# Performance work log

Measured on AMD Instinct MI355X. Metric: run time of the kernel, lower is better.

## Reference

```python
import jax, jax.numpy as jnp
import numpy as np
import math

B, S, D, H = 2, 2048, 1024, 16
DH = D // H  # head_size = 64


def setup_inputs() -> dict:
    key = jax.random.key(0)
    ks = jax.random.split(key, 11)
    s = 0.02
    return {
        "queries": jax.random.normal(ks[0], (B, S, D), jnp.float32),
        "keys": jax.random.normal(ks[1], (B, S, D), jnp.float32),
        "values": jax.random.normal(ks[2], (B, S, D), jnp.float32),
        # nn.Linear weights: y = x @ W.T + b, W has shape (out, in)
        "W_Q": jax.random.normal(ks[3], (D, D), jnp.float32) * s,
        "b_Q": jax.random.normal(ks[4], (D,), jnp.float32) * s,
        "W_K": jax.random.normal(ks[5], (D, D), jnp.float32) * s,
        "b_K": jax.random.normal(ks[6], (D,), jnp.float32) * s,
        "W_V": jax.random.normal(ks[7], (D, D), jnp.float32) * s,
        "b_V": jax.random.normal(ks[8], (D,), jnp.float32) * s,
        "W_O": jax.random.normal(ks[9], (D, D), jnp.float32) * s,
        "b_O": jax.random.normal(ks[10], (D,), jnp.float32) * s,
    }


def _split_heads(x):
    # (B, S, H*DH) -> (B, H, S, DH); torch.chunk+stack == reshape+transpose
    b, s, _ = x.shape
    return x.reshape(b, s, H, DH).transpose(0, 2, 1, 3)


def reference(queries, keys, values, W_Q, b_Q, W_K, b_K, W_V, b_V, W_O, b_O):
    q = _split_heads(queries @ W_Q.T + b_Q)  # (B,H,S,DH)
    k = _split_heads(keys @ W_K.T + b_K)
    v = _split_heads(values @ W_V.T + b_V)

    scale = 1.0 / math.sqrt(DH)
    scores = jnp.einsum("bhqd,bhkd->bhqk", q, k) * scale  # (B,H,S,S)
    causal = jnp.tril(jnp.ones((S, S), dtype=bool))  # allow j <= i (causal)
    scores = jnp.where(causal, scores, -jnp.inf)
    weights = jax.nn.softmax(scores, axis=-1)

    attended = jnp.einsum("bhqk,bhkd->bhqd", weights, v)  # (B,H,S,DH)
    merged = attended.transpose(0, 2, 1, 3).reshape(B, S, D)  # merge_heads
    return merged @ W_O.T + b_O
```

## Files before the change

### kernel.cpp

```cpp
#include <hip/hip_runtime.h>


typedef __bf16 bf16x8 __attribute__((ext_vector_type(8)));
typedef float  f32x4  __attribute__((ext_vector_type(4)));

#define B_  2
#define S_  2048
#define D_  1024
#define H_  16
#define DH_ 64

#define NEG_ 1.0e30f
#define M2_  5.77078016f
#define QSCALE_ 0.18033688f

#if __has_builtin(__builtin_amdgcn_exp2f)
#define EXP2(x) __builtin_amdgcn_exp2f(x)
#else
#define EXP2(x) __builtin_exp2f(x)
#endif

__device__ __forceinline__ void load_lds16(const __bf16* g, __bf16* lds_base) {
    __builtin_amdgcn_global_load_lds(
        (const __attribute__((address_space(1))) void*)g,
        (__attribute__((address_space(3))) void*)lds_base,
        16, 0, 0);
}

__device__ __forceinline__ bf16x8 cvt8(const float* __restrict__ p) {
    const float4 a = *(const float4*)p;
    const float4 b = *(const float4*)(p + 4);
    bf16x8 r;
    r[0] = (__bf16)a.x; r[1] = (__bf16)a.y; r[2] = (__bf16)a.z; r[3] = (__bf16)a.w;
    r[4] = (__bf16)b.x; r[5] = (__bf16)b.y; r[6] = (__bf16)b.z; r[7] = (__bf16)b.w;
    return r;
}

__global__ void cvt_kernel(const float* __restrict__ q, const float* __restrict__ k,
                           const float* __restrict__ v,
                           const float* __restrict__ wq, const float* __restrict__ wk,
                           const float* __restrict__ wv, const float* __restrict__ wo,
                           __bf16* __restrict__ qb, __bf16* __restrict__ kb,
                           __bf16* __restrict__ vb,
                           __bf16* __restrict__ wqb, __bf16* __restrict__ wkb,
                           __bf16* __restrict__ wvb, __bf16* __restrict__ wob) {
    const int z = blockIdx.z;
    const float* src; __bf16* dst; size_t n;
    switch (z) {
        case 0: src = q;  dst = qb;  n = (size_t)B_ * S_ * D_; break;
        case 1: src = k;  dst = kb;  n = (size_t)B_ * S_ * D_; break;
        case 2: src = v;  dst = vb;  n = (size_t)B_ * S_ * D_; break;
        case 3: src = wq; dst = wqb; n = (size_t)D_ * D_; break;
        case 4: src = wk; dst = wkb; n = (size_t)D_ * D_; break;
        case 5: src = wv; dst = wvb; n = (size_t)D_ * D_; break;
        default: src = wo; dst = wob; n = (size_t)D_ * D_; break;
    }
    const size_t i = ((size_t)blockIdx.x * 256 + threadIdx.x) * 8;
    if (i >= n) return;
    *(bf16x8*)(dst + i) = cvt8(src + i);
}

__device__ __forceinline__ void gemm128_bf(const __bf16* __restrict__ X,
                                           const __bf16* __restrict__ W,
                                           int m0, int n0, int K,
                                           __bf16* As, __bf16* Bs,
                                           f32x4 acc[4][4]) {
    const int tid  = threadIdx.x;
    const int wave = tid >> 6, lane = tid & 63;
    const int row  = lane & 15, quad = lane >> 4;
    const int wm   = wave >> 1, wn = wave & 1;
    const int arow = lane >> 2;
    const int acol = (lane & 3) * 8;

    const f32x4 fzero = {0.f, 0.f, 0.f, 0.f};
#pragma unroll
    for (int mt = 0; mt < 4; ++mt)
#pragma unroll
        for (int nt = 0; nt < 4; ++nt) acc[mt][nt] = fzero;

    for (int k0 = 0; k0 < K; k0 += 32) {
#pragma unroll
        for (int c = 0; c < 2; ++c) {
            const int j = wave * 2 + c;
            load_lds16(X + (size_t)(m0 + j * 16 + arow) * K + k0 + acol, As + j * 512);
            load_lds16(W + (size_t)(n0 + j * 16 + arow) * K + k0 + acol, Bs + j * 512);
        }
        __syncthreads();
        bf16x8 af[4], bfv[4];
#pragma unroll
        for (int t = 0; t < 4; ++t) {
            af[t]  = *(const bf16x8*)(As + (wm * 64 + t * 16 + row) * 32 + quad * 8);
            bfv[t] = *(const bf16x8*)(Bs + (wn * 64 + t * 16 + row) * 32 + quad * 8);
        }
#pragma unroll
        for (int mt = 0; mt < 4; ++mt)
#pragma unroll
            for (int nt = 0; nt < 4; ++nt)
                acc[mt][nt] = __builtin_amdgcn_mfma_f32_16x16x32_bf16(
                    af[mt], bfv[nt], acc[mt][nt], 0, 0, 0);
        __syncthreads();
    }
}

__global__ void qkv_kernel(const __bf16* __restrict__ qb, const __bf16* __restrict__ kb,
                           const __bf16* __restrict__ vb,
                           const __bf16* __restrict__ wqb, const __bf16* __restrict__ wkb,
                           const __bf16* __restrict__ wvb,
                           const float* __restrict__ bq, const float* __restrict__ bk,
                           const float* __restrict__ bv,
                           __bf16* __restrict__ q_ws, __bf16* __restrict__ k_ws,
                           __bf16* __restrict__ v_ws) {
    __shared__ __align__(16) __bf16 As[128 * 32];
    __shared__ __align__(16) __bf16 Bs[128 * 32];
    const int mode = blockIdx.z;
    const __bf16* X    = mode == 0 ? qb : mode == 1 ? kb : vb;
    const __bf16* W    = mode == 0 ? wqb : mode == 1 ? wkb : wvb;
    const float*  bias = mode == 0 ? bq : mode == 1 ? bk : bv;
    const int m0 = blockIdx.y * 128, n0 = blockIdx.x * 128;

    f32x4 acc[4][4];
    gemm128_bf(X, W, m0, n0, D_, As, Bs, acc);

    const int tid = threadIdx.x;
    const int wave = tid >> 6, lane = tid & 63;
    const int row = lane & 15, quad = lane >> 4;
    const int wm = wave >> 1, wn = wave & 1;

#pragma unroll
    for (int nt = 0; nt < 4; ++nt) {
        const int n  = n0 + wn * 64 + nt * 16 + row;
        const float bf = bias[n];
        const int h = n >> 6, dh = n & 63;
#pragma unroll
        for (int mt = 0; mt < 4; ++mt) {
#pragma unroll
            for (int r = 0; r < 4; ++r) {
                const int m = m0 + wm * 64 + mt * 16 + quad * 4 + r;
                const int bb = m >> 11, s = m & (S_ - 1);
                const float val = acc[mt][nt][r] + bf;
                if (mode == 0)
                    q_ws[(((size_t)bb * H_ + h) * S_ + s) * DH_ + dh] = (__bf16)(val * QSCALE_);
                else if (mode == 1)
                    k_ws[(((size_t)bb * H_ + h) * S_ + s) * DH_ + dh] = (__bf16)val;
                else
                    v_ws[(((size_t)bb * H_ + h) * DH_ + dh) * S_ + s] = (__bf16)val;
            }
        }
    }
}

__global__ void attn_kernel(const __bf16* __restrict__ q_ws, const __bf16* __restrict__ k_ws,
                            const __bf16* __restrict__ v_ws, __bf16* __restrict__ att) {
    __shared__ __align__(16) __bf16 Ks[128 * 64];
    __shared__ __align__(16) __bf16 Vs[64 * 128];
    __shared__ __align__(16) __bf16 Ps[4 * 32 * 32];

    const int bh = blockIdx.x;
    const int qt = (S_ / 128 - 1) - blockIdx.y;
    const int tid = threadIdx.x, wave = tid >> 6, lane = tid & 63;
    const int row = lane & 15, quad = lane >> 4;

    const __bf16* Qg = q_ws + ((size_t)bh * S_ + qt * 128 + wave * 32) * DH_;
    const __bf16* Kg = k_ws + (size_t)bh * S_ * DH_;
    const __bf16* Vg = v_ws + (size_t)bh * DH_ * S_;
    __bf16* Pw = Ps + wave * 1024;

    bf16x8 qf[2][2];
#pragma unroll
    for (int mt = 0; mt < 2; ++mt)
#pragma unroll
        for (int ks = 0; ks < 2; ++ks)
            qf[mt][ks] = *(const bf16x8*)(Qg + (mt * 16 + row) * DH_ + ks * 32 + quad * 8);

    bf16x8 onesf;
#pragma unroll
    for (int i = 0; i < 8; ++i) onesf[i] = (__bf16)1.0f;

    const f32x4 fzero = {0.f, 0.f, 0.f, 0.f};
    f32x4 oacc[2][4];
    f32x4 lacc[2];
#pragma unroll
    for (int mt = 0; mt < 2; ++mt) {
#pragma unroll
        for (int dt = 0; dt < 4; ++dt) oacc[mt][dt] = fzero;
        lacc[mt] = fzero;
    }

    for (int kv = 0; kv <= qt; ++kv) {
#pragma unroll
        for (int c = 0; c < 4; ++c) {
            const int ck = wave * 4 + c;
            load_lds16(Kg + (size_t)kv * 128 * DH_ + ck * 512 + lane * 8, Ks + ck * 512);
            load_lds16(Vg + (size_t)(ck * 4 + (lane >> 4)) * S_ + kv * 128 + (lane & 15) * 8,
                       Vs + ck * 512);
        }
        __syncthreads();

        const bool diag = (kv == qt);
#pragma unroll
        for (int kc = 0; kc < 4; ++kc) {
            f32x4 s[2][2];
#pragma unroll
            for (int mt = 0; mt < 2; ++mt)
#pragma unroll
                for (int jn = 0; jn < 2; ++jn) s[mt][jn] = fzero;
#pragma unroll
            for (int jn = 0; jn < 2; ++jn) {
                const int nt = kc * 2 + jn;
                bf16x8 kf0 = *(const bf16x8*)(Ks + (nt * 16 + row) * DH_ + quad * 8);
                bf16x8 kf1 = *(const bf16x8*)(Ks + (nt * 16 + row) * DH_ + 32 + quad * 8);
#pragma unroll
                for (int mt = 0; mt < 2; ++mt) {
                    s[mt][jn] = __builtin_amdgcn_mfma_f32_16x16x32_bf16(qf[mt][0], kf0, s[mt][jn], 0, 0, 0);
                    s[mt][jn] = __builtin_amdgcn_mfma_f32_16x16x32_bf16(qf[mt][1], kf1, s[mt][jn], 0, 0, 0);
                }
            }

            if (diag) {
#pragma unroll
                for (int mt = 0; mt < 2; ++mt)
#pragma unroll
                    for (int jn = 0; jn < 2; ++jn) {
                        const int cloc = kc * 32 + jn * 16 + row;
#pragma unroll
                        for (int r = 0; r < 4; ++r) {
                            const int rloc = wave * 32 + mt * 16 + quad * 4 + r;
                            if (cloc > rloc) s[mt][jn][r] = -NEG_;
                        }
                    }
            }

#pragma unroll
            for (int mt = 0; mt < 2; ++mt)
#pragma unroll
                for (int r = 0; r < 4; ++r)
#pragma unroll
                    for (int jn = 0; jn < 2; ++jn) {
                        const float p = EXP2(s[mt][jn][r] - M2_);
                        Pw[(mt * 16 + quad * 4 + r) * 32 + jn * 16 + row] = (__bf16)p;
                    }

            bf16x8 pf0 = *(const bf16x8*)(Pw + (row) * 32 + quad * 8);
            bf16x8 pf1 = *(const bf16x8*)(Pw + (16 + row) * 32 + quad * 8);
#pragma unroll
            for (int dt = 0; dt < 4; ++dt) {
                bf16x8 vf = *(const bf16x8*)(Vs + (dt * 16 + row) * 128 + kc * 32 + quad * 8);
                oacc[0][dt] = __builtin_amdgcn_mfma_f32_16x16x32_bf16(pf0, vf, oacc[0][dt], 0, 0, 0);
                oacc[1][dt] = __builtin_amdgcn_mfma_f32_16x16x32_bf16(pf1, vf, oacc[1][dt], 0, 0, 0);
            }
            lacc[0] = __builtin_amdgcn_mfma_f32_16x16x32_bf16(pf0, onesf, lacc[0], 0, 0, 0);
            lacc[1] = __builtin_amdgcn_mfma_f32_16x16x32_bf16(pf1, onesf, lacc[1], 0, 0, 0);
        }
        __syncthreads();
    }

    const int b = bh >> 4, h = bh & 15;
#pragma unroll
    for (int mt = 0; mt < 2; ++mt) {
#pragma unroll
        for (int r = 0; r < 4; ++r) {
            const float inv = 1.f / lacc[mt][r];
            const int s = qt * 128 + wave * 32 + mt * 16 + quad * 4 + r;
#pragma unroll
            for (int dt = 0; dt < 4; ++dt) {
                att[((size_t)b * S_ + s) * D_ + h * DH_ + dt * 16 + row] =
                    (__bf16)(oacc[mt][dt][r] * inv);
            }
        }
    }
}

__global__ void oproj_kernel(const __bf16* __restrict__ attn, const __bf16* __restrict__ wob,
                             const float* __restrict__ bo, float* __restrict__ out) {
    __shared__ __align__(16) __bf16 As[128 * 32];
    __shared__ __align__(16) __bf16 Bs[128 * 32];
    const int m0 = blockIdx.y * 128, n0 = blockIdx.x * 128;

    f32x4 acc[4][4];
    gemm128_bf(attn, wob, m0, n0, D_, As, Bs, acc);

    const int tid = threadIdx.x;
    const int wave = tid >> 6, lane = tid & 63;
    const int row = lane & 15, quad = lane >> 4;
    const int wm = wave >> 1, wn = wave & 1;

#pragma unroll
    for (int nt = 0; nt < 4; ++nt) {
        const int n = n0 + wn * 64 + nt * 16 + row;
        const float bf = bo[n];
#pragma unroll
        for (int mt = 0; mt < 4; ++mt) {
#pragma unroll
            for (int r = 0; r < 4; ++r) {
                const int m = m0 + wm * 64 + mt * 16 + quad * 4 + r;
                out[(size_t)m * D_ + n] = acc[mt][nt][r] + bf;
            }
        }
    }
}

extern "C" void kernel_launch(void* const* d_in, const int* in_sizes, int n_in,
                              void* d_out, int out_size, void* d_ws, size_t ws_size,
                              hipStream_t stream) {
    const float* q_in = (const float*)d_in[0];
    const float* k_in = (const float*)d_in[1];
    const float* v_in = (const float*)d_in[2];
    const float* wq   = (const float*)d_in[3];
    const float* bq   = (const float*)d_in[4];
    const float* wk   = (const float*)d_in[5];
    const float* bk   = (const float*)d_in[6];
    const float* wv   = (const float*)d_in[7];
    const float* bv   = (const float*)d_in[8];
    const float* wo   = (const float*)d_in[9];
    const float* bo   = (const float*)d_in[10];

    char* ws = (char*)d_ws;
    const size_t MB = 1024 * 1024;
    __bf16* qb   = (__bf16*)(ws);
    __bf16* kb   = (__bf16*)(ws + 8 * MB);
    __bf16* vb   = (__bf16*)(ws + 16 * MB);
    __bf16* wqb  = (__bf16*)(ws + 24 * MB);
    __bf16* wkb  = (__bf16*)(ws + 26 * MB);
    __bf16* wvb  = (__bf16*)(ws + 28 * MB);
    __bf16* wob  = (__bf16*)(ws + 30 * MB);
    __bf16* q_ws = (__bf16*)(ws + 32 * MB);
    __bf16* k_ws = (__bf16*)(ws + 40 * MB);
    __bf16* v_ws = (__bf16*)(ws + 48 * MB);
    __bf16* attb = qb;
    float*  out  = (float*)d_out;

    cvt_kernel<<<dim3(2048, 1, 7), 256, 0, stream>>>(
        q_in, k_in, v_in, wq, wk, wv, wo, qb, kb, vb, wqb, wkb, wvb, wob);
    qkv_kernel<<<dim3(D_ / 128, (B_ * S_) / 128, 3), 256, 0, stream>>>(
        qb, kb, vb, wqb, wkb, wvb, bq, bk, bv, q_ws, k_ws, v_ws);
    attn_kernel<<<dim3(B_ * H_, S_ / 128), 256, 0, stream>>>(q_ws, k_ws, v_ws, attb);
    oproj_kernel<<<dim3(D_ / 128, (B_ * S_) / 128), 256, 0, stream>>>(attb, wob, bo, out);
}
```

Before: 242.6 us.

## Compute transposed scores to keep P in registers and skip masked diagonal tiles

The attention kernel now computes S^T = K·Q^T, so each lane's score fragment maps straight onto the A-operand layout of a 16x16x16 MFMA for P·V. That removes the LDS round-trip for P and the ones-vector MFMA used for row sums; row sums are instead kept as per-lane float accumulators and reduced with shuffles at the end. K and V tiles are staged into padded LDS with 4-byte global_load_lds to avoid bank conflicts. On the diagonal tile each wave processes only the key subtiles its causal mask can reach. The costs are 4x more small LDS-load instructions and a lower-throughput MFMA shape for P·V.

Result: slower. 255.9 us (+5.5%).

```diff
diff --git a/kernel.cpp b/kernel.cpp
--- a/kernel.cpp
+++ b/kernel.cpp
@@ -2,6 +2,8 @@
 
 
 typedef __bf16 bf16x8 __attribute__((ext_vector_type(8)));
+typedef __bf16 bf16x4 __attribute__((ext_vector_type(4)));
+typedef short  s16x4  __attribute__((ext_vector_type(4)));
 typedef float  f32x4  __attribute__((ext_vector_type(4)));
 
 #define B_  2
@@ -20,11 +22,26 @@
 #define EXP2(x) __builtin_exp2f(x)
 #endif
 
+__device__ __forceinline__ f32x4 mfma16x16(bf16x4 a, bf16x4 b, f32x4 c) {
+#if __has_builtin(__builtin_amdgcn_mfma_f32_16x16x16_bf16)
+    return __builtin_amdgcn_mfma_f32_16x16x16_bf16(a, b, c, 0, 0, 0);
+#else
+    return __builtin_amdgcn_mfma_f32_16x16x16bf16_1k(
+        __builtin_bit_cast(s16x4, a), __builtin_bit_cast(s16x4, b), c, 0, 0, 0);
+#endif
+}
+
 __device__ __forceinline__ void load_lds16(const __bf16* g, __bf16* lds_base) {
     __builtin_amdgcn_global_load_lds(
         (const __attribute__((address_space(1))) void*)g,
         (__attribute__((address_space(3))) void*)lds_base,
         16, 0, 0);
+}
+__device__ __forceinline__ void load_lds4(const __bf16* g, __bf16* lds_base) {
+    __builtin_amdgcn_global_load_lds(
+        (const __attribute__((address_space(1))) void*)g,
+        (__attribute__((address_space(3))) void*)lds_base,
+        4, 0, 0);
 }
 
 __device__ __forceinline__ bf16x8 cvt8(const float* __restrict__ p) {
@@ -149,11 +166,12 @@
     }
 }
 
+#define KSTR 136
+#define VSTR 136
 __global__ void attn_kernel(const __bf16* __restrict__ q_ws, const __bf16* __restrict__ k_ws,
                             const __bf16* __restrict__ v_ws, __bf16* __restrict__ att) {
-    __shared__ __align__(16) __bf16 Ks[128 * 64];
-    __shared__ __align__(16) __bf16 Vs[64 * 128];
-    __shared__ __align__(16) __bf16 Ps[4 * 32 * 32];
+    __shared__ __align__(16) __bf16 Ks[64 * KSTR];
+    __shared__ __align__(16) __bf16 Vs[64 * VSTR];
 
     const int bh = blockIdx.x;
     const int qt = (S_ / 128 - 1) - blockIdx.y;
@@ -163,108 +181,97 @@
     const __bf16* Qg = q_ws + ((size_t)bh * S_ + qt * 128 + wave * 32) * DH_;
     const __bf16* Kg = k_ws + (size_t)bh * S_ * DH_;
     const __bf16* Vg = v_ws + (size_t)bh * DH_ * S_;
-    __bf16* Pw = Ps + wave * 1024;
 
     bf16x8 qf[2][2];
 #pragma unroll
-    for (int mt = 0; mt < 2; ++mt)
+    for (int jq = 0; jq < 2; ++jq)
 #pragma unroll
         for (int ks = 0; ks < 2; ++ks)
-            qf[mt][ks] = *(const bf16x8*)(Qg + (mt * 16 + row) * DH_ + ks * 32 + quad * 8);
-
-    bf16x8 onesf;
-#pragma unroll
-    for (int i = 0; i < 8; ++i) onesf[i] = (__bf16)1.0f;
+            qf[jq][ks] = *(const bf16x8*)(Qg + (jq * 16 + row) * DH_ + ks * 32 + quad * 8);
 
     const f32x4 fzero = {0.f, 0.f, 0.f, 0.f};
     f32x4 oacc[2][4];
-    f32x4 lacc[2];
-#pragma unroll
-    for (int mt = 0; mt < 2; ++mt) {
-#pragma unroll
-        for (int dt = 0; dt < 4; ++dt) oacc[mt][dt] = fzero;
-        lacc[mt] = fzero;
-    }
+    float lsum[2] = {0.f, 0.f};
+#pragma unroll
+    for (int jq = 0; jq < 2; ++jq)
+#pragma unroll
+        for (int dt = 0; dt < 4; ++dt) oacc[jq][dt] = fzero;
+
+    const int kfbase = (row >> 1) * KSTR + (row & 1) * 64 + quad * 8;
+    const int vfbase = row * VSTR + quad * 4;
 
     for (int kv = 0; kv <= qt; ++kv) {
 #pragma unroll
-        for (int c = 0; c < 4; ++c) {
-            const int ck = wave * 4 + c;
-            load_lds16(Kg + (size_t)kv * 128 * DH_ + ck * 512 + lane * 8, Ks + ck * 512);
-            load_lds16(Vg + (size_t)(ck * 4 + (lane >> 4)) * S_ + kv * 128 + (lane & 15) * 8,
-                       Vs + ck * 512);
+        for (int c = 0; c < 16; ++c) {
+            const int g = wave * 16 + c;
+            load_lds4(Kg + (size_t)kv * 128 * DH_ + g * 128 + lane * 2, Ks + g * KSTR);
+            load_lds4(Vg + (size_t)g * S_ + kv * 128 + lane * 2, Vs + g * VSTR);
         }
         __syncthreads();
 
         const bool diag = (kv == qt);
-#pragma unroll
-        for (int kc = 0; kc < 4; ++kc) {
-            f32x4 s[2][2];
-#pragma unroll
-            for (int mt = 0; mt < 2; ++mt)
-#pragma unroll
-                for (int jn = 0; jn < 2; ++jn) s[mt][jn] = fzero;
-#pragma unroll
-            for (int jn = 0; jn < 2; ++jn) {
-                const int nt = kc * 2 + jn;
-                bf16x8 kf0 = *(const bf16x8*)(Ks + (nt * 16 + row) * DH_ + quad * 8);
-                bf16x8 kf1 = *(const bf16x8*)(Ks + (nt * 16 + row) * DH_ + 32 + quad * 8);
-#pragma unroll
-                for (int mt = 0; mt < 2; ++mt) {
-                    s[mt][jn] = __builtin_amdgcn_mfma_f32_16x16x32_bf16(qf[mt][0], kf0, s[mt][jn], 0, 0, 0);
-                    s[mt][jn] = __builtin_amdgcn_mfma_f32_16x16x32_bf16(qf[mt][1], kf1, s[mt][jn], 0, 0, 0);
+        const int nkt = diag ? (2 * wave + 2) : 8;
+
+        for (int kt = 0; kt < nkt; ++kt) {
+            bf16x8 kf0 = *(const bf16x8*)(Ks + kfbase + kt * 8 * KSTR);
+            bf16x8 kf1 = *(const bf16x8*)(Ks + kfbase + kt * 8 * KSTR + 32);
+            f32x4 s[2];
+#pragma unroll
+            for (int jq = 0; jq < 2; ++jq) {
+                s[jq] = __builtin_amdgcn_mfma_f32_16x16x32_bf16(kf0, qf[jq][0], fzero, 0, 0, 0);
+                s[jq] = __builtin_amdgcn_mfma_f32_16x16x32_bf16(kf1, qf[jq][1], s[jq], 0, 0, 0);
+            }
+
+            if (diag) {
+#pragma unroll
+                for (int jq = 0; jq < 2; ++jq) {
+                    const int q = wave * 32 + jq * 16 + row;
+#pragma unroll
+                    for (int r = 0; r < 4; ++r) {
+                        const int key = kt * 16 + quad * 4 + r;
+                        if (key > q) s[jq][r] = -NEG_;
+                    }
                 }
             }
 
-            if (diag) {
-#pragma unroll
-                for (int mt = 0; mt < 2; ++mt)
-#pragma unroll
-                    for (int jn = 0; jn < 2; ++jn) {
-                        const int cloc = kc * 32 + jn * 16 + row;
-#pragma unroll
-                        for (int r = 0; r < 4; ++r) {
-                            const int rloc = wave * 32 + mt * 16 + quad * 4 + r;
-                            if (cloc > rloc) s[mt][jn][r] = -NEG_;
-                        }
-                    }
-            }
-
-#pragma unroll
-            for (int mt = 0; mt < 2; ++mt)
-#pragma unroll
-                for (int r = 0; r < 4; ++r)
-#pragma unroll
-                    for (int jn = 0; jn < 2; ++jn) {
-                        const float p = EXP2(s[mt][jn][r] - M2_);
-                        Pw[(mt * 16 + quad * 4 + r) * 32 + jn * 16 + row] = (__bf16)p;
-                    }
-
-            bf16x8 pf0 = *(const bf16x8*)(Pw + (row) * 32 + quad * 8);
-            bf16x8 pf1 = *(const bf16x8*)(Pw + (16 + row) * 32 + quad * 8);
+            bf16x4 pa[2];
+#pragma unroll
+            for (int jq = 0; jq < 2; ++jq) {
+                float ls = lsum[jq];
+#pragma unroll
+                for (int r = 0; r < 4; ++r) {
+                    const float p = EXP2(s[jq][r] - M2_);
+                    ls += p;
+                    pa[jq][r] = (__bf16)p;
+                }
+                lsum[jq] = ls;
+            }
+
 #pragma unroll
             for (int dt = 0; dt < 4; ++dt) {
-                bf16x8 vf = *(const bf16x8*)(Vs + (dt * 16 + row) * 128 + kc * 32 + quad * 8);
-                oacc[0][dt] = __builtin_amdgcn_mfma_f32_16x16x32_bf16(pf0, vf, oacc[0][dt], 0, 0, 0);
-                oacc[1][dt] = __builtin_amdgcn_mfma_f32_16x16x32_bf16(pf1, vf, oacc[1][dt], 0, 0, 0);
-            }
-            lacc[0] = __builtin_amdgcn_mfma_f32_16x16x32_bf16(pf0, onesf, lacc[0], 0, 0, 0);
-            lacc[1] = __builtin_amdgcn_mfma_f32_16x16x32_bf16(pf1, onesf, lacc[1], 0, 0, 0);
+                bf16x4 vf = *(const bf16x4*)(Vs + vfbase + dt * 16 * VSTR + kt * 16);
+                oacc[0][dt] = mfma16x16(pa[0], vf, oacc[0][dt]);
+                oacc[1][dt] = mfma16x16(pa[1], vf, oacc[1][dt]);
+            }
         }
         __syncthreads();
     }
 
     const int b = bh >> 4, h = bh & 15;
 #pragma unroll
-    for (int mt = 0; mt < 2; ++mt) {
+    for (int jq = 0; jq < 2; ++jq) {
+        float ls = lsum[jq];
+        ls += __shfl_xor(ls, 16);
+        ls += __shfl_xor(ls, 32);
 #pragma unroll
         for (int r = 0; r < 4; ++r) {
-            const float inv = 1.f / lacc[mt][r];
-            const int s = qt * 128 + wave * 32 + mt * 16 + quad * 4 + r;
+            const float lv = __shfl(ls, quad * 4 + r);
+            const float inv = 1.f / lv;
+            const int sq = qt * 128 + wave * 32 + jq * 16 + quad * 4 + r;
 #pragma unroll
             for (int dt = 0; dt < 4; ++dt) {
-                att[((size_t)b * S_ + s) * D_ + h * DH_ + dt * 16 + row] =
-                    (__bf16)(oacc[mt][dt][r] * inv);
+                att[((size_t)b * S_ + sq) * D_ + h * DH_ + dt * 16 + row] =
+                    (__bf16)(oacc[jq][dt][r] * inv);
             }
         }
     }
```
